# Performance work log

Hardware: AMD Instinct MI355X
Metric: run time of the kernel (lower is better)

The kernel has to match this reference:

```python
import jax, jax.numpy as jnp
import numpy as np

B, S, K_TAGS = 64, 1024, 64

def setup_inputs() -> dict:
    key = jax.random.key(0)
    k1, k2 = jax.random.split(key)
    # Emissions scaled to mean ~1 and transitions scaled so sum_k A*T stays O(1)
    # (the layer runs the CRF forward pass in probability space, log_space=False,
    #  so unscaled values would underflow over 1024 steps).
    X = jax.random.uniform(k1, (B, S, K_TAGS), dtype=jnp.float32) * 2.0
    T = jax.random.uniform(k2, (K_TAGS, K_TAGS, K_TAGS), dtype=jnp.float32) * (2.0 / K_TAGS)
    return {"X": X, "T": T}

def _crf2_forward(X, T):
    # Second-order CRF forward algorithm (non-log space), returning per-step
    # alpha marginals so output shape == input shape (B, S, K).
    b, s, k = X.shape
    x0 = X[:, 0]  # (B, K)
    # pair-state alpha A[b,i,j]: score of sequences ending in tag pair (i, j)
    A0 = jnp.broadcast_to(x0[:, None, :], (b, k, k)) / k  # sum_i A0 == x0

    def step(A, x_t):
        # A_t[b,i,j] = x_t[b,j] * sum_k A_{t-1}[b,k,i] * T[k,i,j]
        A_new = x_t[:, None, :] * jnp.einsum('bki,kij->bij', A, T)
        return A_new, A_new.sum(axis=1)  # marginal alpha over previous tag

    xs = jnp.swapaxes(X[:, 1:], 0, 1)  # (S-1, B, K) time-major for scan
    _, ys = jax.lax.scan(step, A0, xs)  # ys: (S-1, B, K)
    y = jnp.concatenate([x0[None], ys], axis=0)  # (S, B, K)
    return jnp.swapaxes(y, 0, 1)  # (B, S, K)

def reference(X, T):
    return _crf2_forward(X, T)
```

## Files before the change

### kernel.cpp

```cpp
#include <hip/hip_runtime.h>
#include <cstdint>


typedef _Float16 f16;
typedef _Float16 f16x8 __attribute__((ext_vector_type(8)));
typedef float f32x4 __attribute__((ext_vector_type(4)));
typedef unsigned int u32;
typedef unsigned short u16;
typedef u32 u32x4v __attribute__((ext_vector_type(4)));

#define SLOT_WORDS 262144

static __device__ inline void st_agent(u32* p, u32 v) {
  __hip_atomic_store(p, v, __ATOMIC_RELAXED, __HIP_MEMORY_SCOPE_AGENT);
}
static __device__ inline u32 ld_agent(const u32* p) {
  return __hip_atomic_load(p, __ATOMIC_RELAXED, __HIP_MEMORY_SCOPE_AGENT);
}

static __device__ inline float fdot2_(u32 a, u32 b, float c) {
  typedef _Float16 f16x2 __attribute__((ext_vector_type(2)));
  f16x2 av = __builtin_bit_cast(f16x2, a);
  f16x2 bv = __builtin_bit_cast(f16x2, b);
#if __has_builtin(__builtin_amdgcn_fdot2)
  return __builtin_amdgcn_fdot2(av, bv, c, false);
#else
  c = __builtin_fmaf((float)av[0], (float)bv[0], c);
  return __builtin_fmaf((float)av[1], (float)bv[1], c);
#endif
}

static __device__ inline u32 pack_tag(float v, u32 q) {
  f16 h = (f16)v;
  f16 l = (f16)(v - (float)h);
  u32 hb = (u32)__builtin_bit_cast(u16, h);
  u32 lb = (u32)__builtin_bit_cast(u16, l);
  lb = (lb & 0xFFFEu) | q;
  return hb | (lb << 16);
}

static __device__ inline f16x8 mk8(u32 a, u32 b, u32 c, u32 d) {
  u32x4v t = {a, b, c, d};
  return __builtin_bit_cast(f16x8, t);
}

__global__ void prep_kernel(const float* __restrict__ X, u32* __restrict__ wsA,
                            float* __restrict__ Y) {
  int idx = blockIdx.x * 256 + threadIdx.x;
  wsA[idx] = (idx >> 18) ? 0x00010000u : 0u;
  if (idx < 4096) {
    int b = idx >> 6, j = idx & 63;
    Y[b * 65536 + j] = X[b * 65536 + j];
  }
}

__global__ __launch_bounds__(512, 1)
void crf_kernel(const float* __restrict__ X, const float* __restrict__ Tg,
                u32* __restrict__ wsA, float* __restrict__ Y) {
  __shared__ u32 Aex[4 * 64 * 17];
  __shared__ float yph[4][2][16];

  const int i_me = blockIdx.x;
  const int tid  = threadIdx.x;
  const int w    = tid >> 6;
  const int l    = tid & 63;
  const int lq   = l >> 4;
  const int ln   = l & 15;
  const int mt   = w >> 1;
  const int h    = w & 1;
  const int ntb  = h * 2;

  u32 Bf[2][2][4];
#pragma unroll
  for (int s = 0; s < 2; ++s)
#pragma unroll
    for (int kb = 0; kb < 2; ++kb)
#pragma unroll
      for (int r = 0; r < 4; ++r) {
        int k0 = kb * 32 + lq * 8 + 2 * r;
        int j  = (ntb + s) * 16 + ln;
        f16 a = (f16)Tg[k0 * 4096 + i_me * 64 + j];
        f16 b = (f16)Tg[(k0 + 1) * 4096 + i_me * 64 + j];
        Bf[s][kb][r] = (u32)__builtin_bit_cast(u16, a) |
                       ((u32)__builtin_bit_cast(u16, b) << 16);
      }

  u32 Af[4][4];
  {
    float v = X[(mt * 16 + ln) * 65536 + i_me] * 0.015625f;
    f16 hh = (f16)v; f16 lo = (f16)(v - (float)hh);
    u32 hw = (u32)__builtin_bit_cast(u16, hh);  hw |= hw << 16;
    u32 lw = (u32)__builtin_bit_cast(u16, lo);  lw &= 0xFFFEu; lw |= lw << 16;
#pragma unroll
    for (int r = 0; r < 4; ++r) { Af[0][r] = hw; Af[1][r] = hw; Af[2][r] = lw; Af[3][r] = lw; }
  }

  const int cbase = (h * 32 + lq * 8) * 4096 + mt * 1024 + i_me * 16 + ln;
  const int pbase = (i_me * 4 + mt) * 1024 + ntb * 256 + ln * 16 + lq * 4;

  for (int t = 1; t <= 1024; ++t) {
    float xs[2][4];
    if (t < 1024) {
#pragma unroll
      for (int s = 0; s < 2; ++s)
#pragma unroll
        for (int r = 0; r < 4; ++r)
          xs[s][r] = X[(mt * 16 + lq * 4 + r) * 65536 + t * 64 + (ntb + s) * 16 + ln];
    }

    u32 W[8];
    if (t > 1) {
      const u32 qm = ((u32)(((t - 1) >> 1) & 1)) << 16;
      const u32* sb = wsA + (((t - 1) & 1) ? SLOT_WORDS : 0);
      int guard = 0;
      for (;;) {
        u32 f[8];
#pragma unroll
        for (int e = 0; e < 8; ++e) f[e] = ld_agent(sb + cbase + e * 4096);
        u32 bad = 0;
#pragma unroll
        for (int e = 0; e < 8; ++e) bad |= (f[e] ^ qm) & 0x10000u;
        if (!bad || ++guard > (1 << 20)) {
#pragma unroll
          for (int e = 0; e < 8; ++e) W[e] = f[e];
          break;
        }
      }
      float ys = 0.f;
#pragma unroll
      for (int e = 0; e < 8; ++e) ys = fdot2_(W[e], 0x3C003C00u, ys);
      ys += __shfl_xor(ys, 16);
      ys += __shfl_xor(ys, 32);
      if (l < 16) yph[mt][h][l] = ys;
      if (t < 1024) {
#pragma unroll
        for (int e = 0; e < 8; ++e)
          Aex[(mt * 64 + h * 32 + lq * 8 + e) * 17 + ln] = W[e];
      }
    }

    __syncthreads();

    if (t > 1 && h == 0 && l < 16) {
      float yv = yph[mt][0][l] + yph[mt][1][l];
      st_agent((u32*)(Y + (mt * 16 + l) * 65536 + (t - 1) * 64 + i_me),
               __builtin_bit_cast(u32, yv));
    }
    if (t == 1024) break;

    if (t > 1) {
      u32 V[8];
#pragma unroll
      for (int e = 0; e < 8; ++e)
        V[e] = Aex[(mt * 64 + (1 - h) * 32 + lq * 8 + e) * 17 + ln];
      u32 W0[8], W1[8];
#pragma unroll
      for (int e = 0; e < 8; ++e) { W0[e] = h ? V[e] : W[e]; W1[e] = h ? W[e] : V[e]; }
#pragma unroll
      for (int r = 0; r < 4; ++r) {
        Af[0][r] = __builtin_amdgcn_perm(W0[2 * r + 1], W0[2 * r], 0x05040100u);
        Af[1][r] = __builtin_amdgcn_perm(W1[2 * r + 1], W1[2 * r], 0x05040100u);
        Af[2][r] = __builtin_amdgcn_perm(W0[2 * r + 1], W0[2 * r], 0x07060302u) & 0xFFFEFFFEu;
        Af[3][r] = __builtin_amdgcn_perm(W1[2 * r + 1], W1[2 * r], 0x07060302u) & 0xFFFEFFFEu;
      }
    }

    __syncthreads();

    f16x8 a0 = mk8(Af[0][0], Af[0][1], Af[0][2], Af[0][3]);
    f16x8 a1 = mk8(Af[1][0], Af[1][1], Af[1][2], Af[1][3]);
    f16x8 a2 = mk8(Af[2][0], Af[2][1], Af[2][2], Af[2][3]);
    f16x8 a3 = mk8(Af[3][0], Af[3][1], Af[3][2], Af[3][3]);
    f16x8 b00 = mk8(Bf[0][0][0], Bf[0][0][1], Bf[0][0][2], Bf[0][0][3]);
    f16x8 b01 = mk8(Bf[0][1][0], Bf[0][1][1], Bf[0][1][2], Bf[0][1][3]);
    f16x8 b10 = mk8(Bf[1][0][0], Bf[1][0][1], Bf[1][0][2], Bf[1][0][3]);
    f16x8 b11 = mk8(Bf[1][1][0], Bf[1][1][1], Bf[1][1][2], Bf[1][1][3]);
    f32x4 acc0 = {0.f, 0.f, 0.f, 0.f};
    f32x4 acc1 = {0.f, 0.f, 0.f, 0.f};
    acc0 = __builtin_amdgcn_mfma_f32_16x16x32_f16(a0, b00, acc0, 0, 0, 0);
    acc0 = __builtin_amdgcn_mfma_f32_16x16x32_f16(a1, b01, acc0, 0, 0, 0);
    acc0 = __builtin_amdgcn_mfma_f32_16x16x32_f16(a2, b00, acc0, 0, 0, 0);
    acc0 = __builtin_amdgcn_mfma_f32_16x16x32_f16(a3, b01, acc0, 0, 0, 0);
    acc1 = __builtin_amdgcn_mfma_f32_16x16x32_f16(a0, b10, acc1, 0, 0, 0);
    acc1 = __builtin_amdgcn_mfma_f32_16x16x32_f16(a1, b11, acc1, 0, 0, 0);
    acc1 = __builtin_amdgcn_mfma_f32_16x16x32_f16(a2, b10, acc1, 0, 0, 0);
    acc1 = __builtin_amdgcn_mfma_f32_16x16x32_f16(a3, b11, acc1, 0, 0, 0);

    const u32 q = (u32)((t >> 1) & 1);
    u32* sb2 = wsA + ((t & 1) ? SLOT_WORDS : 0);
    u32x4v d0, d1;
#pragma unroll
    for (int r = 0; r < 4; ++r) {
      d0[r] = pack_tag(xs[0][r] * acc0[r], q);
      d1[r] = pack_tag(xs[1][r] * acc1[r], q);
    }
    u32* p0 = sb2 + pbase;
    u32* p1 = p0 + 256;
    asm volatile("global_store_dwordx4 %0, %1, off sc0 sc1" :: "v"(p0), "v"(d0) : "memory");
    asm volatile("global_store_dwordx4 %0, %1, off sc0 sc1" :: "v"(p1), "v"(d1) : "memory");
  }
}

extern "C" void kernel_launch(void* const* d_in, const int* in_sizes, int n_in,
                              void* d_out, int out_size, void* d_ws, size_t ws_size,
                              hipStream_t stream) {
  const float* X = (const float*)d_in[0];
  const float* T = (const float*)d_in[1];
  float* Y = (float*)d_out;
  u32* wsA = (u32*)d_ws;

  prep_kernel<<<2048, 256, 0, stream>>>(X, wsA, Y);
  crf_kernel<<<64, 512, 0, stream>>>(X, T, wsA, Y);
}
```

Baseline: 2.692 ms.

## Load both halves of pair-state directly, drop LDS exchange and a barrier

Each wave now polls and loads both the h=0 and h=1 halves of the previous step's pair-state from global memory itself. This replaces the LDS exchange between paired waves, removes one __syncthreads per step, and computes the output marginal redundantly per wave instead of combining partials through shared memory. The MFMA and store of the next state are moved ahead of the marginal reduction and Y write. The emission loads for the next step are prefetched after the current step's work. In exchange, global polling traffic per wave doubles, and both waves of a pair redundantly reduce the marginal.

Result: faster. 2.175 ms (-19.2%).

```diff
diff --git a/kernel.cpp b/kernel.cpp
--- a/kernel.cpp
+++ b/kernel.cpp
@@ -57,9 +57,6 @@
 __global__ __launch_bounds__(512, 1)
 void crf_kernel(const float* __restrict__ X, const float* __restrict__ Tg,
                 u32* __restrict__ wsA, float* __restrict__ Y) {
-  __shared__ u32 Aex[4 * 64 * 17];
-  __shared__ float yph[4][2][16];
-
   const int i_me = blockIdx.x;
   const int tid  = threadIdx.x;
   const int w    = tid >> 6;
@@ -95,67 +92,46 @@
     for (int r = 0; r < 4; ++r) { Af[0][r] = hw; Af[1][r] = hw; Af[2][r] = lw; Af[3][r] = lw; }
   }
 
-  const int cbase = (h * 32 + lq * 8) * 4096 + mt * 1024 + i_me * 16 + ln;
+  const int cbase = (lq * 8) * 4096 + mt * 1024 + i_me * 16 + ln;
   const int pbase = (i_me * 4 + mt) * 1024 + ntb * 256 + ln * 16 + lq * 4;
 
+  float xs[2][4];
+#pragma unroll
+  for (int s = 0; s < 2; ++s)
+#pragma unroll
+    for (int r = 0; r < 4; ++r)
+      xs[s][r] = X[(mt * 16 + lq * 4 + r) * 65536 + 64 + (ntb + s) * 16 + ln];
+
   for (int t = 1; t <= 1024; ++t) {
-    float xs[2][4];
-    if (t < 1024) {
-#pragma unroll
-      for (int s = 0; s < 2; ++s)
-#pragma unroll
-        for (int r = 0; r < 4; ++r)
-          xs[s][r] = X[(mt * 16 + lq * 4 + r) * 65536 + t * 64 + (ntb + s) * 16 + ln];
-    }
-
-    u32 W[8];
+    u32 W0[8], W1[8];
     if (t > 1) {
       const u32 qm = ((u32)(((t - 1) >> 1) & 1)) << 16;
       const u32* sb = wsA + (((t - 1) & 1) ? SLOT_WORDS : 0);
       int guard = 0;
       for (;;) {
-        u32 f[8];
-#pragma unroll
-        for (int e = 0; e < 8; ++e) f[e] = ld_agent(sb + cbase + e * 4096);
+        u32 f0[8], f1[8];
+#pragma unroll
+        for (int e = 0; e < 8; ++e) {
+          f0[e] = ld_agent(sb + cbase + e * 4096);
+          f1[e] = ld_agent(sb + cbase + e * 4096 + 131072);
+        }
         u32 bad = 0;
 #pragma unroll
-        for (int e = 0; e < 8; ++e) bad |= (f[e] ^ qm) & 0x10000u;
+        for (int e = 0; e < 8; ++e) {
+          bad |= (f0[e] ^ qm) & 0x10000u;
+          bad |= (f1[e] ^ qm) & 0x10000u;
+        }
         if (!bad || ++guard > (1 << 20)) {
 #pragma unroll
-          for (int e = 0; e < 8; ++e) W[e] = f[e];
+          for (int e = 0; e < 8; ++e) { W0[e] = f0[e]; W1[e] = f1[e]; }
           break;
         }
       }
-      float ys = 0.f;
-#pragma unroll
-      for (int e = 0; e < 8; ++e) ys = fdot2_(W[e], 0x3C003C00u, ys);
-      ys += __shfl_xor(ys, 16);
-      ys += __shfl_xor(ys, 32);
-      if (l < 16) yph[mt][h][l] = ys;
-      if (t < 1024) {
-#pragma unroll
-        for (int e = 0; e < 8; ++e)
-          Aex[(mt * 64 + h * 32 + lq * 8 + e) * 17 + ln] = W[e];
-      }
     }
 
     __syncthreads();
 
-    if (t > 1 && h == 0 && l < 16) {
-      float yv = yph[mt][0][l] + yph[mt][1][l];
-      st_agent((u32*)(Y + (mt * 16 + l) * 65536 + (t - 1) * 64 + i_me),
-               __builtin_bit_cast(u32, yv));
-    }
-    if (t == 1024) break;
-
     if (t > 1) {
-      u32 V[8];
-#pragma unroll
-      for (int e = 0; e < 8; ++e)
-        V[e] = Aex[(mt * 64 + (1 - h) * 32 + lq * 8 + e) * 17 + ln];
-      u32 W0[8], W1[8];
-#pragma unroll
-      for (int e = 0; e < 8; ++e) { W0[e] = h ? V[e] : W[e]; W1[e] = h ? W[e] : V[e]; }
 #pragma unroll
       for (int r = 0; r < 4; ++r) {
         Af[0][r] = __builtin_amdgcn_perm(W0[2 * r + 1], W0[2 * r], 0x05040100u);
@@ -165,39 +141,59 @@
       }
     }
 
-    __syncthreads();
-
-    f16x8 a0 = mk8(Af[0][0], Af[0][1], Af[0][2], Af[0][3]);
-    f16x8 a1 = mk8(Af[1][0], Af[1][1], Af[1][2], Af[1][3]);
-    f16x8 a2 = mk8(Af[2][0], Af[2][1], Af[2][2], Af[2][3]);
-    f16x8 a3 = mk8(Af[3][0], Af[3][1], Af[3][2], Af[3][3]);
-    f16x8 b00 = mk8(Bf[0][0][0], Bf[0][0][1], Bf[0][0][2], Bf[0][0][3]);
-    f16x8 b01 = mk8(Bf[0][1][0], Bf[0][1][1], Bf[0][1][2], Bf[0][1][3]);
-    f16x8 b10 = mk8(Bf[1][0][0], Bf[1][0][1], Bf[1][0][2], Bf[1][0][3]);
-    f16x8 b11 = mk8(Bf[1][1][0], Bf[1][1][1], Bf[1][1][2], Bf[1][1][3]);
-    f32x4 acc0 = {0.f, 0.f, 0.f, 0.f};
-    f32x4 acc1 = {0.f, 0.f, 0.f, 0.f};
-    acc0 = __builtin_amdgcn_mfma_f32_16x16x32_f16(a0, b00, acc0, 0, 0, 0);
-    acc0 = __builtin_amdgcn_mfma_f32_16x16x32_f16(a1, b01, acc0, 0, 0, 0);
-    acc0 = __builtin_amdgcn_mfma_f32_16x16x32_f16(a2, b00, acc0, 0, 0, 0);
-    acc0 = __builtin_amdgcn_mfma_f32_16x16x32_f16(a3, b01, acc0, 0, 0, 0);
-    acc1 = __builtin_amdgcn_mfma_f32_16x16x32_f16(a0, b10, acc1, 0, 0, 0);
-    acc1 = __builtin_amdgcn_mfma_f32_16x16x32_f16(a1, b11, acc1, 0, 0, 0);
-    acc1 = __builtin_amdgcn_mfma_f32_16x16x32_f16(a2, b10, acc1, 0, 0, 0);
-    acc1 = __builtin_amdgcn_mfma_f32_16x16x32_f16(a3, b11, acc1, 0, 0, 0);
-
-    const u32 q = (u32)((t >> 1) & 1);
-    u32* sb2 = wsA + ((t & 1) ? SLOT_WORDS : 0);
-    u32x4v d0, d1;
-#pragma unroll
-    for (int r = 0; r < 4; ++r) {
-      d0[r] = pack_tag(xs[0][r] * acc0[r], q);
-      d1[r] = pack_tag(xs[1][r] * acc1[r], q);
-    }
-    u32* p0 = sb2 + pbase;
-    u32* p1 = p0 + 256;
-    asm volatile("global_store_dwordx4 %0, %1, off sc0 sc1" :: "v"(p0), "v"(d0) : "memory");
-    asm volatile("global_store_dwordx4 %0, %1, off sc0 sc1" :: "v"(p1), "v"(d1) : "memory");
+    if (t < 1024) {
+      f16x8 a0 = mk8(Af[0][0], Af[0][1], Af[0][2], Af[0][3]);
+      f16x8 a1 = mk8(Af[1][0], Af[1][1], Af[1][2], Af[1][3]);
+      f16x8 a2 = mk8(Af[2][0], Af[2][1], Af[2][2], Af[2][3]);
+      f16x8 a3 = mk8(Af[3][0], Af[3][1], Af[3][2], Af[3][3]);
+      f16x8 b00 = mk8(Bf[0][0][0], Bf[0][0][1], Bf[0][0][2], Bf[0][0][3]);
+      f16x8 b01 = mk8(Bf[0][1][0], Bf[0][1][1], Bf[0][1][2], Bf[0][1][3]);
+      f16x8 b10 = mk8(Bf[1][0][0], Bf[1][0][1], Bf[1][0][2], Bf[1][0][3]);
+      f16x8 b11 = mk8(Bf[1][1][0], Bf[1][1][1], Bf[1][1][2], Bf[1][1][3]);
+      f32x4 acc0 = {0.f, 0.f, 0.f, 0.f};
+      f32x4 acc1 = {0.f, 0.f, 0.f, 0.f};
+      acc0 = __builtin_amdgcn_mfma_f32_16x16x32_f16(a0, b00, acc0, 0, 0, 0);
+      acc0 = __builtin_amdgcn_mfma_f32_16x16x32_f16(a1, b01, acc0, 0, 0, 0);
+      acc0 = __builtin_amdgcn_mfma_f32_16x16x32_f16(a2, b00, acc0, 0, 0, 0);
+      acc0 = __builtin_amdgcn_mfma_f32_16x16x32_f16(a3, b01, acc0, 0, 0, 0);
+      acc1 = __builtin_amdgcn_mfma_f32_16x16x32_f16(a0, b10, acc1, 0, 0, 0);
+      acc1 = __builtin_amdgcn_mfma_f32_16x16x32_f16(a1, b11, acc1, 0, 0, 0);
+      acc1 = __builtin_amdgcn_mfma_f32_16x16x32_f16(a2, b10, acc1, 0, 0, 0);
+      acc1 = __builtin_amdgcn_mfma_f32_16x16x32_f16(a3, b11, acc1, 0, 0, 0);
+
+      const u32 q = (u32)((t >> 1) & 1);
+      u32* sb2 = wsA + ((t & 1) ? SLOT_WORDS : 0);
+      u32x4v d0, d1;
+#pragma unroll
+      for (int r = 0; r < 4; ++r) {
+        d0[r] = pack_tag(xs[0][r] * acc0[r], q);
+        d1[r] = pack_tag(xs[1][r] * acc1[r], q);
+      }
+      u32* p0 = sb2 + pbase;
+      u32* p1 = p0 + 256;
+      asm volatile("global_store_dwordx4 %0, %1, off sc0 sc1" :: "v"(p0), "v"(d0) : "memory");
+      asm volatile("global_store_dwordx4 %0, %1, off sc0 sc1" :: "v"(p1), "v"(d1) : "memory");
+    }
+
+    if (t > 1) {
+      float ys = 0.f;
+#pragma unroll
+      for (int e = 0; e < 8; ++e) {
+        ys = fdot2_(W0[e], 0x3C003C00u, ys);
+        ys = fdot2_(W1[e], 0x3C003C00u, ys);
+      }
+      ys += __shfl_xor(ys, 16);
+      ys += __shfl_xor(ys, 32);
+      if (h == 0 && l < 16)
+        Y[(mt * 16 + l) * 65536 + (t - 1) * 64 + i_me] = ys;
+    }
+    if (t < 1023) {
+#pragma unroll
+      for (int s = 0; s < 2; ++s)
+#pragma unroll
+        for (int r = 0; r < 4; ++r)
+          xs[s][r] = X[(mt * 16 + lq * 4 + r) * 65536 + (t + 1) * 64 + (ntb + s) * 16 + ln];
+    }
   }
 }
 
```
